# Performance work log

Measured on AMD Instinct MI355X. Metric: run time of the kernel, lower is better.

Reference implementation:

```python
import jax, jax.numpy as jnp
import numpy as np
from jax import lax

B, N, M = 2, 16384, 4096
C1, C2 = 128, 256
H1, H2 = 256, 128  # mlp = [C1+C2, 256, 128]


def setup_inputs() -> dict:
    key = jax.random.key(0)
    ks = jax.random.split(key, 8)
    return {
        "unknown": jax.random.normal(ks[0], (B, N, 3), jnp.float32),
        "known": jax.random.normal(ks[1], (B, M, 3), jnp.float32),
        "unknow_feats": jax.random.normal(ks[2], (B, C1, N), jnp.float32),
        "known_feats": jax.random.normal(ks[3], (B, C2, M), jnp.float32),
        "W1": jax.random.normal(ks[4], (H1, C1 + C2), jnp.float32) * 0.05,
        "b1": jnp.zeros((H1,), jnp.float32),
        "W2": jax.random.normal(ks[5], (H2, H1), jnp.float32) * 0.05,
        "b2": jnp.zeros((H2,), jnp.float32),
    }


def reference(unknown, known, unknow_feats, known_feats, W1, b1, W2, b2):
    # Pairwise squared distances (B, n, m) via ||a||^2 + ||b||^2 - 2 a.b
    d2 = (
        jnp.sum(unknown * unknown, -1)[:, :, None]
        + jnp.sum(known * known, -1)[:, None, :]
        - 2.0 * jnp.einsum("bnd,bmd->bnm", unknown, known)
    )
    # 3 nearest neighbors
    neg_d2, idx = lax.top_k(-d2, 3)  # (B, n, 3)
    dist = jnp.sqrt(jnp.maximum(-neg_d2, 0.0))  # pointops returns sqrt distances
    dist_recip = 1.0 / (dist + 1e-8)
    weight = dist_recip / jnp.sum(dist_recip, axis=2, keepdims=True)  # (B, n, 3)
    # Gather neighbor features (B, C2, n, 3) and inverse-distance weighted sum
    gathered = jax.vmap(lambda f, i: f[:, i])(known_feats, idx)
    interpolated = jnp.sum(gathered * weight[:, None, :, :], axis=-1)  # (B, C2, n)
    new_features = jnp.concatenate([interpolated, unknow_feats], axis=1)  # (B, C1+C2, n)
    # Shared MLP (1x1 convs, bn=False -> conv bias + ReLU)
    h = jax.nn.relu(jnp.einsum("oc,bcn->bon", W1, new_features) + b1[None, :, None])
    out = jax.nn.relu(jnp.einsum("oc,bcn->bon", W2, h) + b2[None, :, None])
    return out  # (B, mlp[-1], n)
```

## Files before the change

kernel.cpp:

```cpp
#include <hip/hip_runtime.h>
#include <hip/hip_bf16.h>

#define BB 2
#define NN 16384
#define MM 4096
#define C1 128
#define C2 256
#define CIN 384
#define H1 256
#define H2 128
#define XROW 392
#define HROW 264

typedef __attribute__((ext_vector_type(8))) short bf16x8;
typedef __attribute__((ext_vector_type(4))) float f32x4;
typedef __attribute__((ext_vector_type(2))) float f32x2;

__device__ __forceinline__ short f32_to_bf16(float x) {
    unsigned u = __float_as_uint(x);
    u += 0x7fffu + ((u >> 16) & 1u);
    return (short)(u >> 16);
}
__device__ __forceinline__ float bf16_to_f32(unsigned short u) {
    union { unsigned u; float f; } c; c.u = ((unsigned)u) << 16; return c.f;
}
__device__ __forceinline__ unsigned pack_bf16x2(float a, float b) {
    __hip_bfloat162 h = __float22bfloat162_rn(make_float2(a, b));
    union { __hip_bfloat162 h; unsigned u; } cv;
    cv.h = h;
    return cv.u;
}
__device__ __forceinline__ f32x2 score2n(f32x2 ax2, f32x2 ay2, f32x2 az2,
                                         f32x2 x, f32x2 y, f32x2 z) {
    f32x2 n = __builtin_elementwise_fma(x, x,
              __builtin_elementwise_fma(y, y, z * z));
    f32x2 t = __builtin_elementwise_fma(az2, z, n);
    t = __builtin_elementwise_fma(ay2, y, t);
    t = __builtin_elementwise_fma(ax2, x, t);
    return t;
}

__global__ __launch_bounds__(256) void prep_kernel(
    const float* __restrict__ KF, unsigned short* __restrict__ KT16,
    const float* __restrict__ W1, const float* __restrict__ W2,
    short* __restrict__ W1b, short* __restrict__ W2b,
    const float* __restrict__ known, float* __restrict__ kxyz)
{
    const int bx  = blockIdx.x;
    const int tid = threadIdx.x;
    if (bx < 2048) {
        __shared__ float tl[32][33];
        const int b  = bx >> 10;
        const int c0 = ((bx >> 7) & 7) * 32;
        const int m0 = (bx & 127) * 32;
        const int tx = tid & 31;
        const int ty = tid >> 5;
        #pragma unroll
        for (int r = 0; r < 4; ++r) {
            int c = ty + r * 8;
            tl[c][tx] = KF[((size_t)b * C2 + c0 + c) * MM + m0 + tx];
        }
        __syncthreads();
        #pragma unroll
        for (int r = 0; r < 4; ++r) {
            int m = ty + r * 8;
            KT16[((size_t)b * MM + m0 + m) * C2 + c0 + tx] =
                (unsigned short)f32_to_bf16(tl[tx][m]);
        }
    } else if (bx < 2432) {
        int i = (bx - 2048) * 256 + tid;
        if (i < H1 * CIN) W1b[i] = f32_to_bf16(W1[i]);
        if (i < H2 * H1)  W2b[i] = f32_to_bf16(W2[i]);
    } else {
        int i = (bx - 2432) * 256 + tid;
        if (i < BB * MM) {
            float x = known[3 * i + 0], y = known[3 * i + 1], z = known[3 * i + 2];
            int b = i >> 12;
            int c = i & (MM - 1);
            int slice = c >> 8;
            int pos   = c & 255;
            float* base = kxyz + (size_t)b * 12288 + slice * 768;
            base[pos] = x; base[256 + pos] = y; base[512 + pos] = z;
        }
    }
}

__global__ __launch_bounds__(1024, 8) void fused_knn_mlp_kernel(
    const float* __restrict__ unknown,
    const float* __restrict__ kxyz,
    const float* __restrict__ unknow_feats,
    const unsigned short* __restrict__ KT16,
    const short* __restrict__ W1b, const float* __restrict__ b1,
    const short* __restrict__ W2b, const float* __restrict__ b2,
    float* __restrict__ out)
{
    __shared__ __align__(16) float candS[12288];
    __shared__ __align__(16) float red[3072];
    __shared__ float vf[64];
    __shared__ int   cnt[64];
    __shared__ int   IsL[64 * 3];
    __shared__ float WsL[64 * 3];

    const int bx    = blockIdx.x;
    const int tid   = threadIdx.x;
    const int lane  = tid & 63;
    const int w     = __builtin_amdgcn_readfirstlane(tid >> 6);
    const int b     = bx >> 8;
    const int qbase = (bx & 255) * 64;
    const int n     = qbase + lane;

    if (tid < 64) cnt[tid] = 0;

    {
        const float* kb = kxyz + (size_t)b * 12288;
        #pragma unroll
        for (int c = 0; c < 3; ++c) {
            const int i = c * 4096 + tid * 4;
            *(f32x4*)&candS[i] = *(const f32x4*)(kb + i);
        }
    }

    {
        const float ux = unknown[((size_t)b * NN + n) * 3 + 0];
        const float uy = unknown[((size_t)b * NN + n) * 3 + 1];
        const float uz = unknown[((size_t)b * NN + n) * 3 + 2];
        const f32x2 ax2 = {-2.f * ux, -2.f * ux};
        const f32x2 ay2 = {-2.f * uy, -2.f * uy};
        const f32x2 az2 = {-2.f * uz, -2.f * uz};

        const float* kw = candS + w * 768;
        __syncthreads();

        float va0 = 3e38f, va1 = 3e38f, va2 = 3e38f;
        float vb0 = 3e38f, vb1 = 3e38f, vb2 = 3e38f;
        unsigned long long mm = 0ull;
        #pragma unroll 2
        for (int t = 0; t < 64; ++t) {
            const f32x4 X = *(const f32x4*)(kw + 4 * t);
            const f32x4 Y = *(const f32x4*)(kw + 256 + 4 * t);
            const f32x4 Z = *(const f32x4*)(kw + 512 + 4 * t);
            const f32x2 xl = {X.x, X.y}, xh = {X.z, X.w};
            const f32x2 yl = {Y.x, Y.y}, yh = {Y.z, Y.w};
            const f32x2 zl = {Z.x, Z.y}, zh = {Z.z, Z.w};
            const f32x2 sl = score2n(ax2, ay2, az2, xl, yl, zl);
            const f32x2 sh = score2n(ax2, ay2, az2, xh, yh, zh);
            bool m0 = sl.x <= va2;
            va2 = __builtin_amdgcn_fmed3f(va1, sl.x, va2);
            va1 = __builtin_amdgcn_fmed3f(va0, sl.x, va1);
            va0 = fminf(sl.x, va0);
            bool m1 = sl.y <= vb2;
            vb2 = __builtin_amdgcn_fmed3f(vb1, sl.y, vb2);
            vb1 = __builtin_amdgcn_fmed3f(vb0, sl.y, vb1);
            vb0 = fminf(sl.y, vb0);
            bool m2 = sh.x <= va2;
            va2 = __builtin_amdgcn_fmed3f(va1, sh.x, va2);
            va1 = __builtin_amdgcn_fmed3f(va0, sh.x, va1);
            va0 = fminf(sh.x, va0);
            bool m3 = sh.y <= vb2;
            vb2 = __builtin_amdgcn_fmed3f(vb1, sh.y, vb2);
            vb1 = __builtin_amdgcn_fmed3f(vb0, sh.y, vb1);
            vb0 = fminf(sh.y, vb0);
            mm |= ((unsigned long long)(m0 | m1 | m2 | m3)) << t;
        }
        {
            float bv[3] = {vb0, vb1, vb2};
            #pragma unroll
            for (int k = 0; k < 3; ++k) {
                float d = bv[k];
                va2 = __builtin_amdgcn_fmed3f(va1, d, va2);
                va1 = __builtin_amdgcn_fmed3f(va0, d, va1);
                va0 = fminf(d, va0);
            }
        }
        red[(w * 64 + lane) * 3 + 0] = va0;
        red[(w * 64 + lane) * 3 + 1] = va1;
        red[(w * 64 + lane) * 3 + 2] = va2;
        __syncthreads();

        if (tid < 64) {
            float r0 = 3e38f, r1 = 3e38f, r2 = 3e38f;
            #pragma unroll
            for (int ww = 0; ww < 16; ++ww) {
                #pragma unroll
                for (int k = 0; k < 3; ++k) {
                    float d = red[(ww * 64 + tid) * 3 + k];
                    r2 = __builtin_amdgcn_fmed3f(r1, d, r2);
                    r1 = __builtin_amdgcn_fmed3f(r0, d, r1);
                    r0 = fminf(d, r0);
                }
            }
            vf[tid] = r2;
        }
        __syncthreads();

        float* mscp = red;
        int*   midp = (int*)red + 512;
        const float v2f = vf[lane];
        unsigned long long m = mm;
        while (m) {
            const int t = (int)__builtin_ctzll(m);
            m &= m - 1;
            const f32x4 X = *(const f32x4*)(kw + 4 * t);
            const f32x4 Y = *(const f32x4*)(kw + 256 + 4 * t);
            const f32x4 Z = *(const f32x4*)(kw + 512 + 4 * t);
            const f32x2 xl = {X.x, X.y}, xh = {X.z, X.w};
            const f32x2 yl = {Y.x, Y.y}, yh = {Y.z, Y.w};
            const f32x2 zl = {Z.x, Z.y}, zh = {Z.z, Z.w};
            const f32x2 sl = score2n(ax2, ay2, az2, xl, yl, zl);
            const f32x2 sh = score2n(ax2, ay2, az2, xh, yh, zh);
            const float sv[4] = {sl.x, sl.y, sh.x, sh.y};
            #pragma unroll
            for (int j = 0; j < 4; ++j) {
                if (sv[j] <= v2f) {
                    int slot = atomicAdd(&cnt[lane], 1);
                    if (slot < 8) {
                        mscp[lane * 8 + slot] = sv[j];
                        midp[lane * 8 + slot] = w * 256 + 4 * t + j;
                    }
                }
            }
        }
        __syncthreads();

        if (tid < 64) {
            const int c = cnt[tid] < 8 ? cnt[tid] : 8;
            float r0 = 3e38f, r1 = 3e38f, r2 = 3e38f;
            int   q0 = 0x7FFFFFFF, q1 = 0x7FFFFFFF, q2 = 0x7FFFFFFF;
            #pragma unroll
            for (int k = 0; k < 8; ++k) {
                float d = (k < c) ? mscp[tid * 8 + k] : 3e38f;
                int   j = (k < c) ? midp[tid * 8 + k] : 0x7FFFFFFF;
                const bool lt0 = (d < r0) || (d == r0 && j < q0);
                const bool lt1 = (d < r1) || (d == r1 && j < q1);
                const bool lt2 = (d < r2) || (d == r2 && j < q2);
                float nr2 = lt1 ? r1 : (lt2 ? d : r2);
                int   nq2 = lt1 ? q1 : (lt2 ? j : q2);
                float nr1 = lt0 ? r0 : (lt1 ? d : r1);
                int   nq1 = lt0 ? q0 : (lt1 ? j : q1);
                float nr0 = lt0 ? d : r0;
                int   nq0 = lt0 ? j : q0;
                r0 = nr0; r1 = nr1; r2 = nr2; q0 = nq0; q1 = nq1; q2 = nq2;
            }
            const float* up = unknown + ((size_t)b * NN + qbase + tid) * 3;
            const float uxx = up[0], uyy = up[1], uzz = up[2];
            const float unq = fmaf(uxx, uxx, fmaf(uyy, uyy, uzz * uzz));
            float d0 = sqrtf(fmaxf(r0 + unq, 0.f));
            float d1 = sqrtf(fmaxf(r1 + unq, 0.f));
            float d2 = sqrtf(fmaxf(r2 + unq, 0.f));
            float i0 = 1.f / (d0 + 1e-8f);
            float i1 = 1.f / (d1 + 1e-8f);
            float i2 = 1.f / (d2 + 1e-8f);
            float s  = i0 + i1 + i2;
            IsL[tid * 3 + 0] = q0; IsL[tid * 3 + 1] = q1; IsL[tid * 3 + 2] = q2;
            WsL[tid * 3 + 0] = i0 / s; WsL[tid * 3 + 1] = i1 / s; WsL[tid * 3 + 2] = i2 / s;
        }
    }
    __syncthreads();

    const unsigned short* KTb = KT16 + (size_t)b * MM * C2;
    short* XH_s = (short*)candS;
    short* Hs_s = (short*)candS + 32 * XROW;
    const int lr = lane & 15;
    const int lq = lane >> 4;
    const int c4 = lane << 2;

    for (int tile = 0; tile < 2; ++tile) {
        const int pbase = tile * 32;

        {
            ushort4 g[2][3];
            #pragma unroll
            for (int j = 0; j < 2; ++j) {
                const int pi = (pbase + 2 * w + j) * 3;
                g[j][0] = *(const ushort4*)(KTb + (size_t)IsL[pi + 0] * C2 + c4);
                g[j][1] = *(const ushort4*)(KTb + (size_t)IsL[pi + 1] * C2 + c4);
                g[j][2] = *(const ushort4*)(KTb + (size_t)IsL[pi + 2] * C2 + c4);
            }
            #pragma unroll
            for (int j = 0; j < 2; ++j) {
                const int pl = 2 * w + j;
                const int pi = (pbase + pl) * 3;
                const float w0 = WsL[pi + 0], w1 = WsL[pi + 1], w2 = WsL[pi + 2];
                float vx = fmaf(w0, bf16_to_f32(g[j][0].x), fmaf(w1, bf16_to_f32(g[j][1].x), w2 * bf16_to_f32(g[j][2].x)));
                float vy = fmaf(w0, bf16_to_f32(g[j][0].y), fmaf(w1, bf16_to_f32(g[j][1].y), w2 * bf16_to_f32(g[j][2].y)));
                float vz = fmaf(w0, bf16_to_f32(g[j][0].z), fmaf(w1, bf16_to_f32(g[j][1].z), w2 * bf16_to_f32(g[j][2].z)));
                float vw = fmaf(w0, bf16_to_f32(g[j][0].w), fmaf(w1, bf16_to_f32(g[j][1].w), w2 * bf16_to_f32(g[j][2].w)));
                uint2 pk;
                pk.x = pack_bf16x2(vx, vy);
                pk.y = pack_bf16x2(vz, vw);
                *(uint2*)&XH_s[pl * XROW + c4] = pk;
            }
            const float* UFb = unknow_feats + (size_t)b * C1 * NN + qbase + pbase;
            const int cc = tid >> 3;
            const int nq = (tid & 7) << 2;
            const float4 f = *(const float4*)(UFb + (size_t)cc * NN + nq);
            XH_s[(nq + 0) * XROW + C2 + cc] = f32_to_bf16(f.x);
            XH_s[(nq + 1) * XROW + C2 + cc] = f32_to_bf16(f.y);
            XH_s[(nq + 2) * XROW + C2 + cc] = f32_to_bf16(f.z);
            XH_s[(nq + 3) * XROW + C2 + cc] = f32_to_bf16(f.w);
        }
        __syncthreads();

        f32x4 acc1[2];
        acc1[0] = (f32x4){0.f, 0.f, 0.f, 0.f};
        acc1[1] = (f32x4){0.f, 0.f, 0.f, 0.f};
        #pragma unroll 4
        for (int k0 = 0; k0 < CIN; k0 += 32) {
            bf16x8 a  = *(const bf16x8*)(W1b + (size_t)(w * 16 + lr) * CIN + k0 + lq * 8);
            bf16x8 x0 = *(bf16x8*)&XH_s[lr * XROW + k0 + lq * 8];
            bf16x8 x1 = *(bf16x8*)&XH_s[(16 + lr) * XROW + k0 + lq * 8];
            acc1[0] = __builtin_amdgcn_mfma_f32_16x16x32_bf16(a, x0, acc1[0], 0, 0, 0);
            acc1[1] = __builtin_amdgcn_mfma_f32_16x16x32_bf16(a, x1, acc1[1], 0, 0, 0);
        }
        {
            const int ob = w * 16 + lq * 4;
            float bb0 = b1[ob + 0], bb1 = b1[ob + 1], bb2 = b1[ob + 2], bb3 = b1[ob + 3];
            #pragma unroll
            for (int p = 0; p < 2; ++p) {
                uint2 pk;
                pk.x = pack_bf16x2(fmaxf(acc1[p].x + bb0, 0.f),
                                   fmaxf(acc1[p].y + bb1, 0.f));
                pk.y = pack_bf16x2(fmaxf(acc1[p].z + bb2, 0.f),
                                   fmaxf(acc1[p].w + bb3, 0.f));
                *(uint2*)&Hs_s[(p * 16 + lr) * HROW + ob] = pk;
            }
        }
        __syncthreads();

        {
            const int r0 = (w & 7) * 16;
            const int pg = (w >> 3) * 16;
            f32x4 acc2 = (f32x4){0.f, 0.f, 0.f, 0.f};
            #pragma unroll 4
            for (int k0 = 0; k0 < H1; k0 += 32) {
                bf16x8 a2 = *(const bf16x8*)(W2b + (size_t)(r0 + lr) * H1 + k0 + lq * 8);
                bf16x8 h  = *(bf16x8*)&Hs_s[(pg + lr) * HROW + k0 + lq * 8];
                acc2 = __builtin_amdgcn_mfma_f32_16x16x32_bf16(a2, h, acc2, 0, 0, 0);
            }
            const int nn = qbase + pbase + pg + lr;
            #pragma unroll
            for (int r = 0; r < 4; ++r) {
                const int o = r0 + lq * 4 + r;
                out[((size_t)b * H2 + o) * NN + nn] =
                    fmaxf(((const float*)&acc2)[r] + b2[o], 0.f);
            }
        }
        __syncthreads();
    }
}

extern "C" void kernel_launch(void* const* d_in, const int* in_sizes, int n_in,
                              void* d_out, int out_size, void* d_ws, size_t ws_size,
                              hipStream_t stream) {
    const float* unknown      = (const float*)d_in[0];
    const float* known        = (const float*)d_in[1];
    const float* unknow_feats = (const float*)d_in[2];
    const float* known_feats  = (const float*)d_in[3];
    const float* W1           = (const float*)d_in[4];
    const float* b1           = (const float*)d_in[5];
    const float* W2           = (const float*)d_in[6];
    const float* b2           = (const float*)d_in[7];
    float* out = (float*)d_out;

    char* ws = (char*)d_ws;
    short*          W1b  = (short*)(ws);
    short*          W2b  = (short*)(ws + 196608);
    float*          kxyz = (float*)(ws + 262144);
    unsigned short* KT16 = (unsigned short*)(ws + 393216);

    prep_kernel<<<2464, 256, 0, stream>>>(
        known_feats, KT16, W1, W2, W1b, W2b, known, kxyz);

    fused_knn_mlp_kernel<<<512, 1024, 0, stream>>>(
        unknown, kxyz, unknow_feats, KT16, W1b, b1, W2b, b2, out);
}
```

Measured before the change: 160.8 us.

## Split fused KNN+MLP kernel into separate KNN and MLP kernels

The single fused kernel is split into a KNN kernel that writes neighbor indices and weights to workspace and an MLP kernel that reads them back to gather features and run the two-layer MLP. Each kernel now holds only the shared memory it needs, which could raise occupancy, most for the MLP phase. The cost is an extra launch plus a global round-trip for the indices and weights, and the two phases can no longer overlap within a block.

```diff
diff --git a/kernel.cpp b/kernel.cpp
--- a/kernel.cpp
+++ b/kernel.cpp
@@ -85,21 +85,16 @@
     }
 }
 
-__global__ __launch_bounds__(1024, 8) void fused_knn_mlp_kernel(
+__global__ __launch_bounds__(1024, 8) void knn_kernel(
     const float* __restrict__ unknown,
     const float* __restrict__ kxyz,
-    const float* __restrict__ unknow_feats,
-    const unsigned short* __restrict__ KT16,
-    const short* __restrict__ W1b, const float* __restrict__ b1,
-    const short* __restrict__ W2b, const float* __restrict__ b2,
-    float* __restrict__ out)
+    int*   __restrict__ idxW,
+    float* __restrict__ wgtW)
 {
     __shared__ __align__(16) float candS[12288];
     __shared__ __align__(16) float red[3072];
     __shared__ float vf[64];
     __shared__ int   cnt[64];
-    __shared__ int   IsL[64 * 3];
-    __shared__ float WsL[64 * 3];
 
     const int bx    = blockIdx.x;
     const int tid   = threadIdx.x;
@@ -120,146 +115,162 @@
         }
     }
 
+    const float ux = unknown[((size_t)b * NN + n) * 3 + 0];
+    const float uy = unknown[((size_t)b * NN + n) * 3 + 1];
+    const float uz = unknown[((size_t)b * NN + n) * 3 + 2];
+    const f32x2 ax2 = {-2.f * ux, -2.f * ux};
+    const f32x2 ay2 = {-2.f * uy, -2.f * uy};
+    const f32x2 az2 = {-2.f * uz, -2.f * uz};
+
+    const float* kw = candS + w * 768;
+    __syncthreads();
+
+    float va0 = 3e38f, va1 = 3e38f, va2 = 3e38f;
+    float vb0 = 3e38f, vb1 = 3e38f, vb2 = 3e38f;
+    unsigned long long mm = 0ull;
+    #pragma unroll 2
+    for (int t = 0; t < 64; ++t) {
+        const f32x4 X = *(const f32x4*)(kw + 4 * t);
+        const f32x4 Y = *(const f32x4*)(kw + 256 + 4 * t);
+        const f32x4 Z = *(const f32x4*)(kw + 512 + 4 * t);
+        const f32x2 xl = {X.x, X.y}, xh = {X.z, X.w};
+        const f32x2 yl = {Y.x, Y.y}, yh = {Y.z, Y.w};
+        const f32x2 zl = {Z.x, Z.y}, zh = {Z.z, Z.w};
+        const f32x2 sl = score2n(ax2, ay2, az2, xl, yl, zl);
+        const f32x2 sh = score2n(ax2, ay2, az2, xh, yh, zh);
+        bool m0 = sl.x <= va2;
+        va2 = __builtin_amdgcn_fmed3f(va1, sl.x, va2);
+        va1 = __builtin_amdgcn_fmed3f(va0, sl.x, va1);
+        va0 = fminf(sl.x, va0);
+        bool m1 = sl.y <= vb2;
+        vb2 = __builtin_amdgcn_fmed3f(vb1, sl.y, vb2);
+        vb1 = __builtin_amdgcn_fmed3f(vb0, sl.y, vb1);
+        vb0 = fminf(sl.y, vb0);
+        bool m2 = sh.x <= va2;
+        va2 = __builtin_amdgcn_fmed3f(va1, sh.x, va2);
+        va1 = __builtin_amdgcn_fmed3f(va0, sh.x, va1);
+        va0 = fminf(sh.x, va0);
+        bool m3 = sh.y <= vb2;
+        vb2 = __builtin_amdgcn_fmed3f(vb1, sh.y, vb2);
+        vb1 = __builtin_amdgcn_fmed3f(vb0, sh.y, vb1);
+        vb0 = fminf(sh.y, vb0);
+        mm |= ((unsigned long long)(m0 | m1 | m2 | m3)) << t;
+    }
     {
-        const float ux = unknown[((size_t)b * NN + n) * 3 + 0];
-        const float uy = unknown[((size_t)b * NN + n) * 3 + 1];
-        const float uz = unknown[((size_t)b * NN + n) * 3 + 2];
-        const f32x2 ax2 = {-2.f * ux, -2.f * ux};
-        const f32x2 ay2 = {-2.f * uy, -2.f * uy};
-        const f32x2 az2 = {-2.f * uz, -2.f * uz};
-
-        const float* kw = candS + w * 768;
-        __syncthreads();
-
-        float va0 = 3e38f, va1 = 3e38f, va2 = 3e38f;
-        float vb0 = 3e38f, vb1 = 3e38f, vb2 = 3e38f;
-        unsigned long long mm = 0ull;
-        #pragma unroll 2
-        for (int t = 0; t < 64; ++t) {
-            const f32x4 X = *(const f32x4*)(kw + 4 * t);
-            const f32x4 Y = *(const f32x4*)(kw + 256 + 4 * t);
-            const f32x4 Z = *(const f32x4*)(kw + 512 + 4 * t);
-            const f32x2 xl = {X.x, X.y}, xh = {X.z, X.w};
-            const f32x2 yl = {Y.x, Y.y}, yh = {Y.z, Y.w};
-            const f32x2 zl = {Z.x, Z.y}, zh = {Z.z, Z.w};
-            const f32x2 sl = score2n(ax2, ay2, az2, xl, yl, zl);
-            const f32x2 sh = score2n(ax2, ay2, az2, xh, yh, zh);
-            bool m0 = sl.x <= va2;
-            va2 = __builtin_amdgcn_fmed3f(va1, sl.x, va2);
-            va1 = __builtin_amdgcn_fmed3f(va0, sl.x, va1);
-            va0 = fminf(sl.x, va0);
-            bool m1 = sl.y <= vb2;
-            vb2 = __builtin_amdgcn_fmed3f(vb1, sl.y, vb2);
-            vb1 = __builtin_amdgcn_fmed3f(vb0, sl.y, vb1);
-            vb0 = fminf(sl.y, vb0);
-            bool m2 = sh.x <= va2;
-            va2 = __builtin_amdgcn_fmed3f(va1, sh.x, va2);
-            va1 = __builtin_amdgcn_fmed3f(va0, sh.x, va1);
-            va0 = fminf(sh.x, va0);
-            bool m3 = sh.y <= vb2;
-            vb2 = __builtin_amdgcn_fmed3f(vb1, sh.y, vb2);
-            vb1 = __builtin_amdgcn_fmed3f(vb0, sh.y, vb1);
-            vb0 = fminf(sh.y, vb0);
-            mm |= ((unsigned long long)(m0 | m1 | m2 | m3)) << t;
-        }
-        {
-            float bv[3] = {vb0, vb1, vb2};
+        float bv[3] = {vb0, vb1, vb2};
+        #pragma unroll
+        for (int k = 0; k < 3; ++k) {
+            float d = bv[k];
+            va2 = __builtin_amdgcn_fmed3f(va1, d, va2);
+            va1 = __builtin_amdgcn_fmed3f(va0, d, va1);
+            va0 = fminf(d, va0);
+        }
+    }
+    red[(w * 64 + lane) * 3 + 0] = va0;
+    red[(w * 64 + lane) * 3 + 1] = va1;
+    red[(w * 64 + lane) * 3 + 2] = va2;
+    __syncthreads();
+
+    if (tid < 64) {
+        float r0 = 3e38f, r1 = 3e38f, r2 = 3e38f;
+        #pragma unroll
+        for (int ww = 0; ww < 16; ++ww) {
             #pragma unroll
             for (int k = 0; k < 3; ++k) {
-                float d = bv[k];
-                va2 = __builtin_amdgcn_fmed3f(va1, d, va2);
-                va1 = __builtin_amdgcn_fmed3f(va0, d, va1);
-                va0 = fminf(d, va0);
-            }
-        }
-        red[(w * 64 + lane) * 3 + 0] = va0;
-        red[(w * 64 + lane) * 3 + 1] = va1;
-        red[(w * 64 + lane) * 3 + 2] = va2;
-        __syncthreads();
-
-        if (tid < 64) {
-            float r0 = 3e38f, r1 = 3e38f, r2 = 3e38f;
-            #pragma unroll
-            for (int ww = 0; ww < 16; ++ww) {
-                #pragma unroll
-                for (int k = 0; k < 3; ++k) {
-                    float d = red[(ww * 64 + tid) * 3 + k];
-                    r2 = __builtin_amdgcn_fmed3f(r1, d, r2);
-                    r1 = __builtin_amdgcn_fmed3f(r0, d, r1);
-                    r0 = fminf(d, r0);
+                float d = red[(ww * 64 + tid) * 3 + k];
+                r2 = __builtin_amdgcn_fmed3f(r1, d, r2);
+                r1 = __builtin_amdgcn_fmed3f(r0, d, r1);
+                r0 = fminf(d, r0);
+            }
+        }
+        vf[tid] = r2;
+    }
+    __syncthreads();
+
+    float* mscp = red;
+    int*   midp = (int*)red + 512;
+    const float v2f = vf[lane];
+    unsigned long long m = mm;
+    while (m) {
+        const int t = (int)__builtin_ctzll(m);
+        m &= m - 1;
+        const f32x4 X = *(const f32x4*)(kw + 4 * t);
+        const f32x4 Y = *(const f32x4*)(kw + 256 + 4 * t);
+        const f32x4 Z = *(const f32x4*)(kw + 512 + 4 * t);
+        const f32x2 xl = {X.x, X.y}, xh = {X.z, X.w};
+        const f32x2 yl = {Y.x, Y.y}, yh = {Y.z, Y.w};
+        const f32x2 zl = {Z.x, Z.y}, zh = {Z.z, Z.w};
+        const f32x2 sl = score2n(ax2, ay2, az2, xl, yl, zl);
+        const f32x2 sh = score2n(ax2, ay2, az2, xh, yh, zh);
+        const float sv[4] = {sl.x, sl.y, sh.x, sh.y};
+        #pragma unroll
+        for (int j = 0; j < 4; ++j) {
+            if (sv[j] <= v2f) {
+                int slot = atomicAdd(&cnt[lane], 1);
+                if (slot < 8) {
+                    mscp[lane * 8 + slot] = sv[j];
+                    midp[lane * 8 + slot] = w * 256 + 4 * t + j;
                 }
             }
-            vf[tid] = r2;
-        }
-        __syncthreads();
-
-        float* mscp = red;
-        int*   midp = (int*)red + 512;
-        const float v2f = vf[lane];
-        unsigned long long m = mm;
-        while (m) {
-            const int t = (int)__builtin_ctzll(m);
-            m &= m - 1;
-            const f32x4 X = *(const f32x4*)(kw + 4 * t);
-            const f32x4 Y = *(const f32x4*)(kw + 256 + 4 * t);
-            const f32x4 Z = *(const f32x4*)(kw + 512 + 4 * t);
-            const f32x2 xl = {X.x, X.y}, xh = {X.z, X.w};
-            const f32x2 yl = {Y.x, Y.y}, yh = {Y.z, Y.w};
-            const f32x2 zl = {Z.x, Z.y}, zh = {Z.z, Z.w};
-            const f32x2 sl = score2n(ax2, ay2, az2, xl, yl, zl);
-            const f32x2 sh = score2n(ax2, ay2, az2, xh, yh, zh);
-            const float sv[4] = {sl.x, sl.y, sh.x, sh.y};
-            #pragma unroll
-            for (int j = 0; j < 4; ++j) {
-                if (sv[j] <= v2f) {
-                    int slot = atomicAdd(&cnt[lane], 1);
-                    if (slot < 8) {
-                        mscp[lane * 8 + slot] = sv[j];
-                        midp[lane * 8 + slot] = w * 256 + 4 * t + j;
-                    }
-                }
-            }
-        }
-        __syncthreads();
-
-        if (tid < 64) {
-            const int c = cnt[tid] < 8 ? cnt[tid] : 8;
-            float r0 = 3e38f, r1 = 3e38f, r2 = 3e38f;
-            int   q0 = 0x7FFFFFFF, q1 = 0x7FFFFFFF, q2 = 0x7FFFFFFF;
-            #pragma unroll
-            for (int k = 0; k < 8; ++k) {
-                float d = (k < c) ? mscp[tid * 8 + k] : 3e38f;
-                int   j = (k < c) ? midp[tid * 8 + k] : 0x7FFFFFFF;
-                const bool lt0 = (d < r0) || (d == r0 && j < q0);
-                const bool lt1 = (d < r1) || (d == r1 && j < q1);
-                const bool lt2 = (d < r2) || (d == r2 && j < q2);
-                float nr2 = lt1 ? r1 : (lt2 ? d : r2);
-                int   nq2 = lt1 ? q1 : (lt2 ? j : q2);
-                float nr1 = lt0 ? r0 : (lt1 ? d : r1);
-                int   nq1 = lt0 ? q0 : (lt1 ? j : q1);
-                float nr0 = lt0 ? d : r0;
-                int   nq0 = lt0 ? j : q0;
-                r0 = nr0; r1 = nr1; r2 = nr2; q0 = nq0; q1 = nq1; q2 = nq2;
-            }
-            const float* up = unknown + ((size_t)b * NN + qbase + tid) * 3;
-            const float uxx = up[0], uyy = up[1], uzz = up[2];
-            const float unq = fmaf(uxx, uxx, fmaf(uyy, uyy, uzz * uzz));
-            float d0 = sqrtf(fmaxf(r0 + unq, 0.f));
-            float d1 = sqrtf(fmaxf(r1 + unq, 0.f));
-            float d2 = sqrtf(fmaxf(r2 + unq, 0.f));
-            float i0 = 1.f / (d0 + 1e-8f);
-            float i1 = 1.f / (d1 + 1e-8f);
-            float i2 = 1.f / (d2 + 1e-8f);
-            float s  = i0 + i1 + i2;
-            IsL[tid * 3 + 0] = q0; IsL[tid * 3 + 1] = q1; IsL[tid * 3 + 2] = q2;
-            WsL[tid * 3 + 0] = i0 / s; WsL[tid * 3 + 1] = i1 / s; WsL[tid * 3 + 2] = i2 / s;
         }
     }
     __syncthreads();
 
+    if (tid < 64) {
+        const int c = cnt[tid] < 8 ? cnt[tid] : 8;
+        float r0 = 3e38f, r1 = 3e38f, r2 = 3e38f;
+        int   q0 = 0x7FFFFFFF, q1 = 0x7FFFFFFF, q2 = 0x7FFFFFFF;
+        #pragma unroll
+        for (int k = 0; k < 8; ++k) {
+            float d = (k < c) ? mscp[tid * 8 + k] : 3e38f;
+            int   j = (k < c) ? midp[tid * 8 + k] : 0x7FFFFFFF;
+            const bool lt0 = (d < r0) || (d == r0 && j < q0);
+            const bool lt1 = (d < r1) || (d == r1 && j < q1);
+            const bool lt2 = (d < r2) || (d == r2 && j < q2);
+            float nr2 = lt1 ? r1 : (lt2 ? d : r2);
+            int   nq2 = lt1 ? q1 : (lt2 ? j : q2);
+            float nr1 = lt0 ? r0 : (lt1 ? d : r1);
+            int   nq1 = lt0 ? q0 : (lt1 ? j : q1);
+            float nr0 = lt0 ? d : r0;
+            int   nq0 = lt0 ? j : q0;
+            r0 = nr0; r1 = nr1; r2 = nr2; q0 = nq0; q1 = nq1; q2 = nq2;
+        }
+        const float* up = unknown + ((size_t)b * NN + qbase + tid) * 3;
+        const float uxx = up[0], uyy = up[1], uzz = up[2];
+        const float unq = fmaf(uxx, uxx, fmaf(uyy, uyy, uzz * uzz));
+        float d0 = sqrtf(fmaxf(r0 + unq, 0.f));
+        float d1 = sqrtf(fmaxf(r1 + unq, 0.f));
+        float d2 = sqrtf(fmaxf(r2 + unq, 0.f));
+        float i0 = 1.f / (d0 + 1e-8f);
+        float i1 = 1.f / (d1 + 1e-8f);
+        float i2 = 1.f / (d2 + 1e-8f);
+        float s  = i0 + i1 + i2;
+        const size_t o = ((size_t)b * NN + qbase + tid) * 3;
+        idxW[o + 0] = q0; idxW[o + 1] = q1; idxW[o + 2] = q2;
+        wgtW[o + 0] = i0 / s; wgtW[o + 1] = i1 / s; wgtW[o + 2] = i2 / s;
+    }
+}
+
+__global__ __launch_bounds__(1024, 8) void mlp_kernel(
+    const int*   __restrict__ idxW,
+    const float* __restrict__ wgtW,
+    const float* __restrict__ unknow_feats,
+    const unsigned short* __restrict__ KT16,
+    const short* __restrict__ W1b, const float* __restrict__ b1,
+    const short* __restrict__ W2b, const float* __restrict__ b2,
+    float* __restrict__ out)
+{
+    __shared__ short XH_s[32 * XROW];
+    __shared__ short Hs_s[32 * HROW];
+
+    const int bx    = blockIdx.x;
+    const int tid   = threadIdx.x;
+    const int lane  = tid & 63;
+    const int w     = __builtin_amdgcn_readfirstlane(tid >> 6);
+    const int b     = bx >> 8;
+    const int qbase = (bx & 255) * 64;
+
     const unsigned short* KTb = KT16 + (size_t)b * MM * C2;
-    short* XH_s = (short*)candS;
-    short* Hs_s = (short*)candS + 32 * XROW;
     const int lr = lane & 15;
     const int lq = lane >> 4;
     const int c4 = lane << 2;
@@ -268,19 +279,25 @@
         const int pbase = tile * 32;
 
         {
+            int   I[2][3];
+            float W[2][3];
+            #pragma unroll
+            for (int j = 0; j < 2; ++j) {
+                const size_t o = ((size_t)b * NN + qbase + pbase + 2 * w + j) * 3;
+                I[j][0] = idxW[o + 0]; I[j][1] = idxW[o + 1]; I[j][2] = idxW[o + 2];
+                W[j][0] = wgtW[o + 0]; W[j][1] = wgtW[o + 1]; W[j][2] = wgtW[o + 2];
+            }
             ushort4 g[2][3];
             #pragma unroll
             for (int j = 0; j < 2; ++j) {
-                const int pi = (pbase + 2 * w + j) * 3;
-                g[j][0] = *(const ushort4*)(KTb + (size_t)IsL[pi + 0] * C2 + c4);
-                g[j][1] = *(const ushort4*)(KTb + (size_t)IsL[pi + 1] * C2 + c4);
-                g[j][2] = *(const ushort4*)(KTb + (size_t)IsL[pi + 2] * C2 + c4);
+                g[j][0] = *(const ushort4*)(KTb + (size_t)I[j][0] * C2 + c4);
+                g[j][1] = *(const ushort4*)(KTb + (size_t)I[j][1] * C2 + c4);
+                g[j][2] = *(const ushort4*)(KTb + (size_t)I[j][2] * C2 + c4);
             }
             #pragma unroll
             for (int j = 0; j < 2; ++j) {
                 const int pl = 2 * w + j;
-                const int pi = (pbase + pl) * 3;
-                const float w0 = WsL[pi + 0], w1 = WsL[pi + 1], w2 = WsL[pi + 2];
+                const float w0 = W[j][0], w1 = W[j][1], w2 = W[j][2];
                 float vx = fmaf(w0, bf16_to_f32(g[j][0].x), fmaf(w1, bf16_to_f32(g[j][1].x), w2 * bf16_to_f32(g[j][2].x)));
                 float vy = fmaf(w0, bf16_to_f32(g[j][0].y), fmaf(w1, bf16_to_f32(g[j][1].y), w2 * bf16_to_f32(g[j][2].y)));
                 float vz = fmaf(w0, bf16_to_f32(g[j][0].z), fmaf(w1, bf16_to_f32(g[j][1].z), w2 * bf16_to_f32(g[j][2].z)));
@@ -367,10 +384,14 @@
     short*          W2b  = (short*)(ws + 196608);
     float*          kxyz = (float*)(ws + 262144);
     unsigned short* KT16 = (unsigned short*)(ws + 393216);
+    int*            idxW = (int*)(ws + 4587520);
+    float*          wgtW = (float*)(ws + 4980736);
 
     prep_kernel<<<2464, 256, 0, stream>>>(
         known_feats, KT16, W1, W2, W1b, W2b, known, kxyz);
 
-    fused_knn_mlp_kernel<<<512, 1024, 0, stream>>>(
-        unknown, kxyz, unknow_feats, KT16, W1b, b1, W2b, b2, out);
-}
+    knn_kernel<<<512, 1024, 0, stream>>>(unknown, kxyz, idxW, wgtW);
+
+    mlp_kernel<<<512, 1024, 0, stream>>>(
+        idxW, wgtW, unknow_feats, KT16, W1b, b1, W2b, b2, out);
+}
```

Result: slower. 180.5 us (+12.3%).
